# Optimization experiments

Hardware: AMD Instinct MI355X
Metric: run time of the kernel (lower is better)

## Reference

```python
import jax, jax.numpy as jnp
import numpy as np

N = 20000   # nodes
D = 64      # emb_dim
H = 512     # 8 * emb_dim
E = 320000  # edges per graph


def setup_inputs() -> dict:
    key = jax.random.key(0)
    ks = jax.random.split(key, 40)
    i = iter(range(40))
    def nrm(shape, s=0.05):
        return jax.random.normal(ks[next(i)], shape, dtype=jnp.float32) * s
    def edges():
        return jax.random.randint(ks[next(i)], (E,), 0, N, dtype=jnp.int32)
    inp = {}
    inp['k_emb'] = nrm((N, D), 1.0)
    inp['pr_src'] = edges(); inp['pr_dst'] = edges()
    inp['pr_ew'] = jax.random.uniform(ks[next(i)], (E,), dtype=jnp.float32)
    inp['cc_src'] = edges(); inp['cc_dst'] = edges()
    inp['cc_ew'] = jax.random.uniform(ks[next(i)], (E,), dtype=jnp.float32)
    inp['sps_src'] = edges(); inp['sps_dst'] = edges()
    inp['pr_Ws0'] = nrm((D, H)); inp['pr_Wn0'] = nrm((D, H)); inp['pr_b0'] = jnp.zeros((H,), jnp.float32)
    inp['pr_Ws1'] = nrm((H, D)); inp['pr_Wn1'] = nrm((H, D)); inp['pr_b1'] = jnp.zeros((D,), jnp.float32)
    inp['cc_Ws0'] = nrm((D, H)); inp['cc_Wn0'] = nrm((D, H)); inp['cc_b0'] = jnp.zeros((H,), jnp.float32)
    inp['cc_Ws1'] = nrm((H, D)); inp['cc_Wn1'] = nrm((H, D)); inp['cc_b1'] = jnp.zeros((D,), jnp.float32)
    inp['ap_Ws0'] = nrm((D, D)); inp['ap_Wn0'] = nrm((D, D)); inp['ap_b0'] = jnp.zeros((D,), jnp.float32)
    inp['ap_Ws1'] = nrm((D, D)); inp['ap_Wn1'] = nrm((D, D)); inp['ap_b1'] = jnp.zeros((D,), jnp.float32)
    inp['att_W'] = nrm((D, D)); inp['att_b'] = jnp.zeros((D,), jnp.float32)
    return inp


def _sage(x, src, dst, ew, Ws, Wn, b):
    # DGL SAGEConv 'mean': neigh = sum(w_e * h_src) / in_degree; out = x@Ws + neigh@Wn + b
    msg = x[src]                                  # [E, din] gather
    if ew is not None:
        msg = msg * ew[:, None]
    agg = jax.ops.segment_sum(msg, dst, num_segments=N)            # [N, din]
    deg = jax.ops.segment_sum(jnp.ones((msg.shape[0],), x.dtype), dst, num_segments=N)
    agg = agg / jnp.maximum(deg, 1.0)[:, None]
    return x @ Ws + agg @ Wn + b


def reference(k_emb, pr_src, pr_dst, pr_ew, cc_src, cc_dst, cc_ew, sps_src, sps_dst,
              pr_Ws0, pr_Wn0, pr_b0, pr_Ws1, pr_Wn1, pr_b1,
              cc_Ws0, cc_Wn0, cc_b0, cc_Ws1, cc_Wn1, cc_b1,
              ap_Ws0, ap_Wn0, ap_b0, ap_Ws1, ap_Wn1, ap_b1,
              att_W, att_b):
    pr = jax.nn.relu(_sage(k_emb, pr_src, pr_dst, pr_ew, pr_Ws0, pr_Wn0, pr_b0))
    pr = _sage(pr, pr_src, pr_dst, pr_ew, pr_Ws1, pr_Wn1, pr_b1)            # [N, D]
    cc = jax.nn.relu(_sage(k_emb, cc_src, cc_dst, cc_ew, cc_Ws0, cc_Wn0, cc_b0))
    cc = _sage(cc, cc_src, cc_dst, cc_ew, cc_Ws1, cc_Wn1, cc_b1)            # [N, D]
    ap = jax.nn.relu(_sage(k_emb, sps_src, sps_dst, None, ap_Ws0, ap_Wn0, ap_b0))
    ap = _sage(ap, sps_src, sps_dst, None, ap_Ws1, ap_Wn1, ap_b1)           # [N, D]
    # APATT fusion
    z = jnp.stack((pr, cc), axis=1)                      # [N, 2, D]
    proj = jnp.tanh(z @ att_W + att_b)                   # [N, 2, D]
    w = jnp.sum(ap[:, None, :] * proj, axis=-1, keepdims=True).mean(0)  # [2, 1]
    beta = jax.nn.softmax(w, axis=0)                     # [2, 1]
    return (beta * z).sum(axis=1)                        # [N, D]
```

## Files before the change

### kernel.cpp

```cpp
#include <hip/hip_runtime.h>
#include <hip/hip_fp16.h>

#define NN 20000
#define NP 20032
#define DD 64
#define HH 512
#define EE 320000
#define ATT_BLOCKS 625
#define BLOCKS_E (EE / 256)
#define CB 157
#define EPB 4096
#define B1_BLOCKS ((EE + EPB - 1) / EPB)
#define ZERO_N (3 * NN + 3 * CB)
#define ZERO_BLOCKS ((ZERO_N + 255) / 256)

typedef __attribute__((ext_vector_type(8))) short short8;
typedef __attribute__((ext_vector_type(4))) float f32x4;

__device__ __forceinline__ ushort f2bf(float f) {
    union { float f; unsigned u; } v; v.f = f;
    unsigned r = v.u + 0x7FFF + ((v.u >> 16) & 1);
    return (ushort)(r >> 16);
}
__device__ __forceinline__ float bf2f(ushort h) {
    union { unsigned u; float f; } v; v.u = ((unsigned)h) << 16;
    return v.f;
}
__device__ __forceinline__ float ew_of(uint w) {
    __half h = __ushort_as_half((ushort)(w >> 16));
    return __half2float(h);
}

__global__ __launch_bounds__(256) void hist3(const int* __restrict__ d0,
                                             const int* __restrict__ d1,
                                             const int* __restrict__ d2,
                                             int* __restrict__ cnt) {
    int g = blockIdx.x / BLOCKS_E;
    int e = (blockIdx.x % BLOCKS_E) * 256 + threadIdx.x;
    const int* d = (g == 0) ? d0 : (g == 1) ? d1 : d2;
    if (e < EE) atomicAdd(&cnt[g * NN + d[e]], 1);
}

__global__ __launch_bounds__(1024) void scan_kernel(const int* __restrict__ cnt,
                                                    int* __restrict__ rowptr,
                                                    float* __restrict__ invd) {
    __shared__ int part[1024];
    int g = blockIdx.x;
    const int* c = cnt + g * NN;
    int* rp = rowptr + g * (NN + 1);
    int tid = threadIdx.x;
    const int CH = (NN + 1023) / 1024;
    int i0 = tid * CH;
    int s = 0;
    for (int i = 0; i < CH; ++i) { int idx = i0 + i; if (idx < NN) s += c[idx]; }
    part[tid] = s;
    __syncthreads();
    for (int off = 1; off < 1024; off <<= 1) {
        int v = (tid >= off) ? part[tid - off] : 0;
        __syncthreads();
        part[tid] += v;
        __syncthreads();
    }
    int run = (tid > 0) ? part[tid - 1] : 0;
    for (int i = 0; i < CH; ++i) {
        int idx = i0 + i;
        if (idx < NN) {
            int cv = c[idx];
            rp[idx] = run; run += cv;
            invd[g * NN + idx] = 1.0f / fmaxf((float)cv, 1.0f);
        }
    }
    if (tid == 1023) rp[NN] = part[1023];
}

__global__ __launch_bounds__(256) void bucket_coarse(
    const int* __restrict__ s0, const int* __restrict__ d0, const float* __restrict__ w0,
    const int* __restrict__ s1, const int* __restrict__ d1, const float* __restrict__ w1,
    const int* __restrict__ s2, const int* __restrict__ d2,
    const int* __restrict__ rowptr,
    int* __restrict__ ccur,
    uint* __restrict__ ce,
    ushort* __restrict__ cd) {
    __shared__ int cnt_s[CB];
    __shared__ int off_s[CB];
    __shared__ int pos_s[CB];
    __shared__ int gbase[CB];
    __shared__ uint lword[EPB];
    __shared__ ushort ldst[EPB];
    int g = blockIdx.x / B1_BLOCKS;
    int blk = blockIdx.x % B1_BLOCKS;
    const int* S = (g == 0) ? s0 : (g == 1) ? s1 : s2;
    const int* D = (g == 0) ? d0 : (g == 1) ? d1 : d2;
    const float* W = (g == 0) ? w0 : (g == 1) ? w1 : nullptr;
    int e0 = blk * EPB;
    int n = min(EPB, EE - e0);
    for (int i = threadIdx.x; i < CB; i += 256) cnt_s[i] = 0;
    __syncthreads();
    for (int i = threadIdx.x; i < n; i += 256)
        atomicAdd(&cnt_s[D[e0 + i] >> 7], 1);
    __syncthreads();
    if (threadIdx.x == 0) {
        int run = 0;
        for (int i = 0; i < CB; ++i) { off_s[i] = run; run += cnt_s[i]; }
    }
    __syncthreads();
    if (threadIdx.x < CB) pos_s[threadIdx.x] = off_s[threadIdx.x];
    __syncthreads();
    for (int i = threadIdx.x; i < n; i += 256) {
        int e = e0 + i;
        int d = D[e];
        int p = atomicAdd(&pos_s[d >> 7], 1);
        ushort ewh = (g < 2) ? __half_as_ushort(__float2half(W[e])) : 0;
        lword[p] = ((uint)ewh << 16) | (uint)(S[e] & 0xFFFF);
        ldst[p] = (ushort)d;
    }
    __syncthreads();
    if (threadIdx.x < CB)
        gbase[threadIdx.x] = atomicAdd(&ccur[g * CB + threadIdx.x], cnt_s[threadIdx.x]);
    __syncthreads();
    const int* rp = rowptr + g * (NN + 1);
    for (int j = threadIdx.x; j < n; j += 256) {
        ushort d = ldst[j];
        int cb = d >> 7;
        int gpos = rp[cb << 7] + gbase[cb] + (j - off_s[cb]);
        ce[(size_t)g * EE + gpos] = lword[j];
        cd[(size_t)g * EE + gpos] = d;
    }
}

__global__ __launch_bounds__(256) void bucket_fine(
    const int* __restrict__ rowptr,
    const uint* __restrict__ ce, const ushort* __restrict__ cd,
    uint* __restrict__ edge_s,
    ushort* __restrict__ src_s2) {
    __shared__ int rp_s[129];
    __shared__ int cur_s[128];
    int g = blockIdx.x / CB;
    int cb = blockIdx.x % CB;
    const int* rp = rowptr + g * (NN + 1);
    int n0 = cb << 7;
    int n1 = min(n0 + 128, NN);
    int m = n1 - n0;
    if (threadIdx.x <= m) rp_s[threadIdx.x] = rp[n0 + threadIdx.x];
    if (threadIdx.x < m) cur_s[threadIdx.x] = 0;
    __syncthreads();
    int beg = rp_s[0], end = rp_s[m];
    for (int j = beg + threadIdx.x; j < end; j += 256) {
        uint e = ce[(size_t)g * EE + j];
        int dl = (int)cd[(size_t)g * EE + j] - n0;
        int pos = rp_s[dl] + atomicAdd(&cur_s[dl], 1);
        if (g < 2) edge_s[(size_t)g * EE + pos] = e;
        else src_s2[pos] = (ushort)(e & 0xFFFF);
    }
}

__global__ __launch_bounds__(256) void pull_cast3(const ushort* __restrict__ xh,
                                                  const int* __restrict__ rowptr,
                                                  const uint* __restrict__ edge_s,
                                                  const ushort* __restrict__ src_s2,
                                                  const float* __restrict__ invd,
                                                  ushort* __restrict__ aggh) {
    int wid = (blockIdx.x * 256 + threadIdx.x) >> 6;
    int lane = threadIdx.x & 63;
    if (wid >= 3 * NN) return;
    int g = wid / NN, n = wid % NN;
    const int* rp = rowptr + g * (NN + 1);
    int beg = rp[n], end = rp[n + 1];
    int q = lane >> 4, fl = lane & 15;
    float a0 = 0.f, a1 = 0.f, a2 = 0.f, a3 = 0.f;
    for (int i = beg; i < end; i += 4) {
        int e = i + q;
        bool valid = e < end;
        int s; float w;
        if (g < 2) {
            uint ew = valid ? edge_s[(size_t)g * EE + e] : 0u;
            s = (int)(ew & 0xFFFF);
            w = valid ? ew_of(ew) : 0.f;
        } else {
            s = valid ? (int)src_s2[e] : 0;
            w = valid ? 1.f : 0.f;
        }
        ushort4 v = *(const ushort4*)(xh + (size_t)s * DD + fl * 4);
        a0 = fmaf(bf2f(v.x), w, a0);
        a1 = fmaf(bf2f(v.y), w, a1);
        a2 = fmaf(bf2f(v.z), w, a2);
        a3 = fmaf(bf2f(v.w), w, a3);
    }
    a0 += __shfl_xor(a0, 16); a0 += __shfl_xor(a0, 32);
    a1 += __shfl_xor(a1, 16); a1 += __shfl_xor(a1, 32);
    a2 += __shfl_xor(a2, 16); a2 += __shfl_xor(a2, 32);
    a3 += __shfl_xor(a3, 16); a3 += __shfl_xor(a3, 32);
    if (q == 0) {
        float sc = invd[g * NN + n];
        ushort4 o;
        o.x = f2bf(a0 * sc); o.y = f2bf(a1 * sc); o.z = f2bf(a2 * sc); o.w = f2bf(a3 * sc);
        *(ushort4*)(aggh + ((size_t)g * NP + n) * 64 + fl * 4) = o;
    }
}

__global__ __launch_bounds__(256) void pull_combine3(const ushort* __restrict__ xnh,
                                                     const int* __restrict__ rowptr,
                                                     const uint* __restrict__ edge_s,
                                                     const ushort* __restrict__ src_s2,
                                                     const float* __restrict__ invd,
                                                     const float* __restrict__ b_pr,
                                                     const float* __restrict__ b_cc,
                                                     const float* __restrict__ b_ap,
                                                     float* __restrict__ o_pr,
                                                     float* __restrict__ o_cc,
                                                     float* __restrict__ o_ap) {
    int wid = (blockIdx.x * 256 + threadIdx.x) >> 6;
    int lane = threadIdx.x & 63;
    if (wid >= 3 * NN) return;
    int g = wid / NN, n = wid % NN;
    const int* rp = rowptr + g * (NN + 1);
    const ushort* x = xnh + (size_t)g * NP * 64;
    int beg = rp[n], end = rp[n + 1];
    int q = lane >> 4, fl = lane & 15;
    float a0 = 0.f, a1 = 0.f, a2 = 0.f, a3 = 0.f;
    for (int i = beg; i < end; i += 4) {
        int e = i + q;
        bool valid = e < end;
        int s; float w;
        if (g < 2) {
            uint ew = valid ? edge_s[(size_t)g * EE + e] : 0u;
            s = (int)(ew & 0xFFFF);
            w = valid ? ew_of(ew) : 0.f;
        } else {
            s = valid ? (int)src_s2[e] : 0;
            w = valid ? 1.f : 0.f;
        }
        ushort4 v = *(const ushort4*)(x + (size_t)s * DD + fl * 4);
        a0 = fmaf(bf2f(v.x), w, a0);
        a1 = fmaf(bf2f(v.y), w, a1);
        a2 = fmaf(bf2f(v.z), w, a2);
        a3 = fmaf(bf2f(v.w), w, a3);
    }
    a0 += __shfl_xor(a0, 16); a0 += __shfl_xor(a0, 32);
    a1 += __shfl_xor(a1, 16); a1 += __shfl_xor(a1, 32);
    a2 += __shfl_xor(a2, 16); a2 += __shfl_xor(a2, 32);
    a3 += __shfl_xor(a3, 16); a3 += __shfl_xor(a3, 32);
    if (q == 0) {
        float sc = invd[g * NN + n];
        const float* bias = (g == 0) ? b_pr : (g == 1) ? b_cc : b_ap;
        float* out = (g == 0) ? o_pr : (g == 1) ? o_cc : o_ap;
        float4 ov = *(float4*)(out + (size_t)n * DD + fl * 4);
        float4 bv = *(const float4*)(bias + fl * 4);
        ov.x += a0 * sc + bv.x;
        ov.y += a1 * sc + bv.y;
        ov.z += a2 * sc + bv.z;
        ov.w += a3 * sc + bv.w;
        *(float4*)(out + (size_t)n * DD + fl * 4) = ov;
    }
}

__global__ __launch_bounds__(256) void pack_all(
    const float* __restrict__ pr_Ws0, const float* __restrict__ pr_Wn0,
    const float* __restrict__ cc_Ws0, const float* __restrict__ cc_Wn0,
    const float* __restrict__ pr_Ws1, const float* __restrict__ pr_Wn1,
    const float* __restrict__ cc_Ws1, const float* __restrict__ cc_Wn1,
    const float* __restrict__ ap_Ws0, const float* __restrict__ ap_Wn0,
    const float* __restrict__ ap_Ws1, const float* __restrict__ ap_Wn1,
    const float* __restrict__ k_emb,
    ushort* __restrict__ W0h_pr, ushort* __restrict__ W0h_cc,
    ushort* __restrict__ W1h_pr, ushort* __restrict__ W1h_cc,
    ushort* __restrict__ W0h_ap, ushort* __restrict__ W1h_ap,
    ushort* __restrict__ xh,
    int* __restrict__ zero_base) {
    int b = blockIdx.x;
    int tid = threadIdx.x;
    if (b < 512) {
        int t = (b & 255) * 256 + tid;
        const float* Ws = (b < 256) ? pr_Ws0 : cc_Ws0;
        const float* Wn = (b < 256) ? pr_Wn0 : cc_Wn0;
        ushort* o = (b < 256) ? W0h_pr : W0h_cc;
        int c = t >> 7, k = t & 127;
        o[t] = f2bf((k < 64) ? Ws[k * 512 + c] : Wn[(k - 64) * 512 + c]);
    } else if (b < 1024) {
        int t = ((b - 512) & 255) * 256 + tid;
        const float* Ws = (b < 768) ? pr_Ws1 : cc_Ws1;
        const float* Wn = (b < 768) ? pr_Wn1 : cc_Wn1;
        ushort* o = (b < 768) ? W1h_pr : W1h_cc;
        int c = t >> 9, k = t & 511;
        o[t] = f2bf((c < 64) ? Ws[k * 64 + c] : Wn[k * 64 + (c - 64)]);
    } else if (b < 1056) {
        int t = (b - 1024) * 256 + tid;
        int c = t >> 7, k = t & 127;
        W0h_ap[t] = f2bf((k < 64) ? ap_Ws0[k * 64 + c] : ap_Wn0[(k - 64) * 64 + c]);
    } else if (b < 1088) {
        int t = (b - 1056) * 256 + tid;
        int c = t >> 6, k = t & 63;
        W1h_ap[t] = f2bf((c < 64) ? ap_Ws1[k * 64 + c] : ap_Wn1[k * 64 + (c - 64)]);
    } else if (b < 1088 + ZERO_BLOCKS) {
        int t = (b - 1088) * 256 + tid;
        if (t < ZERO_N) zero_base[t] = 0;
    } else {
        int t = (b - 1088 - ZERO_BLOCKS) * 256 + tid;
        if (t < NN * DD) xh[t] = f2bf(k_emb[t]);
    }
}

__global__ __launch_bounds__(512, 4) void fused_sage4(
    const ushort* __restrict__ xh,
    const ushort* __restrict__ aggA,
    const ushort* __restrict__ W0a, const ushort* __restrict__ W1a,
    const ushort* __restrict__ W0b, const ushort* __restrict__ W1b,
    const float* __restrict__ b0a, const float* __restrict__ b0b,
    float* __restrict__ outS0, float* __restrict__ outS1,
    ushort* __restrict__ xnh, int nblk) {
    constexpr int LROW = 136;
    __shared__ ushort Ahs[64 * LROW];
    __shared__ ushort h1s[64 * LROW];
    int br = blockIdx.x / nblk;
    int rb = blockIdx.x % nblk;
    const ushort* W0 = br ? W0b : W0a;
    const ushort* W1 = br ? W1b : W1a;
    const float* b0 = br ? b0b : b0a;
    float* outS = br ? outS1 : outS0;
    ushort* outX = xnh + (size_t)br * NP * 64;
    const ushort* agg = aggA + (size_t)br * NP * 64;
    int row0 = rb * 64;

    int wv = threadIdx.x >> 6;
    int lane = threadIdx.x & 63;
    int lrow = lane & 15;
    int koff = (lane >> 4) * 8;
    int crow = (lane >> 4) * 4;

    {
        int r = threadIdx.x >> 3;
        int seg = threadIdx.x & 7;
        const ushort* src = (seg < 4) ? (xh + (size_t)(row0 + r) * 64 + seg * 16)
                                      : (agg + (size_t)(row0 + r) * 64 + (seg - 4) * 16);
        *(short8*)&Ahs[r * LROW + seg * 16] = *(const short8*)src;
        *(short8*)&Ahs[r * LROW + seg * 16 + 8] = *(const short8*)(src + 8);
    }
    __syncthreads();

    f32x4 C[4] = {};
#pragma unroll
    for (int p = 0; p < 4; ++p) {
        {
            short8 B[4];
#pragma unroll
            for (int kk = 0; kk < 4; ++kk)
                B[kk] = *(const short8*)(W0 + (size_t)(p * 128 + wv * 16 + lrow) * 128 + kk * 32 + koff);
            f32x4 acc[4] = {};
#pragma unroll
            for (int rg = 0; rg < 4; ++rg) {
#pragma unroll
                for (int kk = 0; kk < 4; ++kk) {
                    short8 a = *(const short8*)&Ahs[(rg * 16 + lrow) * LROW + kk * 32 + koff];
                    acc[rg] = __builtin_amdgcn_mfma_f32_16x16x32_bf16(a, B[kk], acc[rg], 0, 0, 0);
                }
            }
            float bb = b0[p * 128 + wv * 16 + lrow];
#pragma unroll
            for (int rg = 0; rg < 4; ++rg) {
#pragma unroll
                for (int r = 0; r < 4; ++r) {
                    float v = fmaxf(acc[rg][r] + bb, 0.0f);
                    h1s[(rg * 16 + crow + r) * LROW + wv * 16 + lrow] = f2bf(v);
                }
            }
        }
        __syncthreads();
        {
            short8 B[4];
#pragma unroll
            for (int kc = 0; kc < 4; ++kc)
                B[kc] = *(const short8*)(W1 + (size_t)(wv * 16 + lrow) * HH + p * 128 + kc * 32 + koff);
#pragma unroll
            for (int rg = 0; rg < 4; ++rg) {
#pragma unroll
                for (int kc = 0; kc < 4; ++kc) {
                    short8 a = *(const short8*)&h1s[(rg * 16 + lrow) * LROW + kc * 32 + koff];
                    C[rg] = __builtin_amdgcn_mfma_f32_16x16x32_bf16(a, B[kc], C[rg], 0, 0, 0);
                }
            }
        }
        __syncthreads();
    }
    int col = wv * 16 + lrow;
    if (col < 64) {
        float* o = outS + col;
#pragma unroll
        for (int rg = 0; rg < 4; ++rg)
#pragma unroll
            for (int r = 0; r < 4; ++r) {
                int row = row0 + rg * 16 + crow + r;
                if (row < NN) o[(size_t)row * 64] = C[rg][r];
            }
    } else {
        ushort* o = outX + (col - 64);
#pragma unroll
        for (int rg = 0; rg < 4; ++rg)
#pragma unroll
            for (int r = 0; r < 4; ++r) {
                int row = row0 + rg * 16 + crow + r;
                if (row < NN) o[(size_t)row * 64] = f2bf(C[rg][r]);
            }
    }
}

__global__ __launch_bounds__(256, 4) void fused_sage_ap(
    const ushort* __restrict__ xh,
    const ushort* __restrict__ agg,
    const ushort* __restrict__ W0,
    const ushort* __restrict__ W1,
    const float* __restrict__ b0,
    float* __restrict__ outS,
    ushort* __restrict__ outX) {
    constexpr int LROW = 72;
    __shared__ ushort h1s[16 * LROW];
    int wv = threadIdx.x >> 6;
    int lane = threadIdx.x & 63;
    int lrow = lane & 15;
    int koff = (lane >> 4) * 8;
    int crow = (lane >> 4) * 4;
    int row0 = blockIdx.x * 16;

    {
        const size_t aoff = (size_t)(row0 + lrow) * 64 + koff;
        short8 aF[4];
#pragma unroll
        for (int kk = 0; kk < 2; ++kk) {
            aF[kk]     = *(const short8*)(xh + aoff + kk * 32);
            aF[2 + kk] = *(const short8*)(agg + aoff + kk * 32);
        }
        f32x4 acc = {};
#pragma unroll
        for (int kk = 0; kk < 4; ++kk) {
            short8 b = *(const short8*)(W0 + (size_t)(wv * 16 + lrow) * 128 + kk * 32 + koff);
            acc = __builtin_amdgcn_mfma_f32_16x16x32_bf16(aF[kk], b, acc, 0, 0, 0);
        }
        float bb = b0[wv * 16 + lrow];
#pragma unroll
        for (int r = 0; r < 4; ++r) {
            h1s[(crow + r) * LROW + wv * 16 + lrow] = f2bf(fmaxf(acc[r] + bb, 0.0f));
        }
    }
    __syncthreads();
    {
        f32x4 C2[2] = {};
#pragma unroll
        for (int kc = 0; kc < 2; ++kc) {
            short8 a = *(const short8*)&h1s[lrow * LROW + kc * 32 + koff];
#pragma unroll
            for (int c = 0; c < 2; ++c) {
                short8 b = *(const short8*)(W1 + (size_t)(wv * 32 + c * 16 + lrow) * 64 + kc * 32 + koff);
                C2[c] = __builtin_amdgcn_mfma_f32_16x16x32_bf16(a, b, C2[c], 0, 0, 0);
            }
        }
#pragma unroll
        for (int c = 0; c < 2; ++c) {
            int col = wv * 32 + c * 16 + lrow;
#pragma unroll
            for (int r = 0; r < 4; ++r) {
                int row = row0 + crow + r;
                if (row < NN) {
                    if (col < 64) outS[(size_t)row * 64 + col] = C2[c][r];
                    else outX[(size_t)row * 64 + (col - 64)] = f2bf(C2[c][r]);
                }
            }
        }
    }
}

__global__ __launch_bounds__(256) void att_stage1(const float* __restrict__ pr,
                                                  const float* __restrict__ cc,
                                                  const float* __restrict__ ap,
                                                  const float* __restrict__ attW,
                                                  const float* __restrict__ attb,
                                                  float2* __restrict__ partial) {
    __shared__ float red[8];
    int lane = threadIdx.x & 63;
    int wv = threadIdx.x >> 6;
    int gw = blockIdx.x * 4 + wv;
    const int nwaves = ATT_BLOCKS * 4;
    float b = attb[lane];
    float c0 = 0.f, c1 = 0.f;
    for (int n = gw; n < NN; n += nwaves) {
        float p0 = 0.f, p1 = 0.f;
        for (int k = 0; k < DD; ++k) {
            float w = attW[k * DD + lane];
            p0 = fmaf(pr[n * DD + k], w, p0);
            p1 = fmaf(cc[n * DD + k], w, p1);
        }
        float a = ap[n * DD + lane];
        c0 += a * tanhf(p0 + b);
        c1 += a * tanhf(p1 + b);
    }
#pragma unroll
    for (int off = 32; off; off >>= 1) {
        c0 += __shfl_xor(c0, off);
        c1 += __shfl_xor(c1, off);
    }
    if (lane == 0) { red[wv * 2] = c0; red[wv * 2 + 1] = c1; }
    __syncthreads();
    if (threadIdx.x == 0) {
        partial[blockIdx.x] = make_float2(red[0] + red[2] + red[4] + red[6],
                                          red[1] + red[3] + red[5] + red[7]);
    }
}

__global__ __launch_bounds__(64) void att_stage2(const float2* __restrict__ partial,
                                                 float* __restrict__ w_acc) {
    int lane = threadIdx.x;
    float s0 = 0.f, s1 = 0.f;
    for (int i = lane; i < ATT_BLOCKS; i += 64) {
        float2 p = partial[i];
        s0 += p.x; s1 += p.y;
    }
#pragma unroll
    for (int off = 32; off; off >>= 1) {
        s0 += __shfl_xor(s0, off);
        s1 += __shfl_xor(s1, off);
    }
    if (lane == 0) { w_acc[0] = s0; w_acc[1] = s1; }
}

__global__ __launch_bounds__(256) void final_kernel(float* __restrict__ pr_out,
                                                    const float* __restrict__ cc,
                                                    const float* __restrict__ w_acc) {
    int t = blockIdx.x * blockDim.x + threadIdx.x;
    if (t >= NN * DD) return;
    float w0 = w_acc[0] * (1.0f / NN);
    float w1 = w_acc[1] * (1.0f / NN);
    float m = fmaxf(w0, w1);
    float e0 = __expf(w0 - m), e1 = __expf(w1 - m);
    float inv = 1.0f / (e0 + e1);
    pr_out[t] = (e0 * pr_out[t] + e1 * cc[t]) * inv;
}

extern "C" void kernel_launch(void* const* d_in, const int* in_sizes, int n_in,
                              void* d_out, int out_size, void* d_ws, size_t ws_size,
                              hipStream_t stream) {
    const float* k_emb  = (const float*)d_in[0];
    const int*   pr_src = (const int*)d_in[1];
    const int*   pr_dst = (const int*)d_in[2];
    const float* pr_ew  = (const float*)d_in[3];
    const int*   cc_src = (const int*)d_in[4];
    const int*   cc_dst = (const int*)d_in[5];
    const float* cc_ew  = (const float*)d_in[6];
    const int*   sps_src = (const int*)d_in[7];
    const int*   sps_dst = (const int*)d_in[8];
    const float* pr_Ws0 = (const float*)d_in[9];
    const float* pr_Wn0 = (const float*)d_in[10];
    const float* pr_b0  = (const float*)d_in[11];
    const float* pr_Ws1 = (const float*)d_in[12];
    const float* pr_Wn1 = (const float*)d_in[13];
    const float* pr_b1  = (const float*)d_in[14];
    const float* cc_Ws0 = (const float*)d_in[15];
    const float* cc_Wn0 = (const float*)d_in[16];
    const float* cc_b0  = (const float*)d_in[17];
    const float* cc_Ws1 = (const float*)d_in[18];
    const float* cc_Wn1 = (const float*)d_in[19];
    const float* cc_b1  = (const float*)d_in[20];
    const float* ap_Ws0 = (const float*)d_in[21];
    const float* ap_Wn0 = (const float*)d_in[22];
    const float* ap_b0  = (const float*)d_in[23];
    const float* ap_Ws1 = (const float*)d_in[24];
    const float* ap_Wn1 = (const float*)d_in[25];
    const float* ap_b1  = (const float*)d_in[26];
    const float* att_W  = (const float*)d_in[27];
    const float* att_b  = (const float*)d_in[28];
    float* out = (float*)d_out;

    char* base = (char*)d_ws;
    size_t off = 0;
    auto alloc = [&](size_t bytes) -> void* {
        void* p = base + off;
        off = (off + bytes + 255) & ~(size_t)255;
        return p;
    };
    float*  invd   = (float*)alloc((size_t)3 * NN * 4);
    int*    cnt    = (int*)alloc((size_t)ZERO_N * 4);
    int*    ccur   = cnt + 3 * NN;
    int*    rowptr = (int*)alloc((size_t)3 * (NN + 1) * 4);
    uint*   edge_s = (uint*)alloc((size_t)2 * EE * 4);
    ushort* src_s2 = (ushort*)alloc((size_t)EE * 2);
    uint*   ce     = (uint*)alloc((size_t)3 * EE * 4);
    ushort* cd     = (ushort*)alloc((size_t)3 * EE * 2);
    float*  w_acc  = (float*)alloc(64);
    float2* att_partial = (float2*)alloc(ATT_BLOCKS * 8);
    ushort* xnh    = (ushort*)alloc((size_t)3 * NP * DD * 2);
    float*  out_cc = (float*)alloc((size_t)NN * DD * 4);
    float*  out_ap = (float*)alloc((size_t)NN * DD * 4);
    ushort* xh     = (ushort*)alloc((size_t)NP * DD * 2);
    ushort* aggh   = (ushort*)alloc((size_t)3 * NP * DD * 2);
    ushort* W0h_pr = (ushort*)alloc(512 * 128 * 2);
    ushort* W0h_cc = (ushort*)alloc(512 * 128 * 2);
    ushort* W0h_ap = (ushort*)alloc(64 * 128 * 2);
    ushort* W1h_pr = (ushort*)alloc(128 * 512 * 2);
    ushort* W1h_cc = (ushort*)alloc(128 * 512 * 2);
    ushort* W1h_ap = (ushort*)alloc(128 * 64 * 2);
    float*  out_pr = out;

    const int TB = 256;
    const int blocks_ND = (NN * DD) / TB;
    const int blocks_pull = (3 * NN * 64) / TB;
    const int NBLK64 = NP / 64;

    pack_all<<<1088 + ZERO_BLOCKS + blocks_ND, TB, 0, stream>>>(
        pr_Ws0, pr_Wn0, cc_Ws0, cc_Wn0, pr_Ws1, pr_Wn1, cc_Ws1, cc_Wn1,
        ap_Ws0, ap_Wn0, ap_Ws1, ap_Wn1, k_emb,
        W0h_pr, W0h_cc, W1h_pr, W1h_cc, W0h_ap, W1h_ap, xh, cnt);

    hist3<<<3 * BLOCKS_E, TB, 0, stream>>>(pr_dst, cc_dst, sps_dst, cnt);
    scan_kernel<<<3, 1024, 0, stream>>>(cnt, rowptr, invd);
    bucket_coarse<<<3 * B1_BLOCKS, TB, 0, stream>>>(pr_src, pr_dst, pr_ew,
                                                    cc_src, cc_dst, cc_ew,
                                                    sps_src, sps_dst,
                                                    rowptr, ccur, ce, cd);
    bucket_fine<<<3 * CB, TB, 0, stream>>>(rowptr, ce, cd, edge_s, src_s2);

    pull_cast3<<<blocks_pull, TB, 0, stream>>>(xh, rowptr, edge_s, src_s2, invd, aggh);

    fused_sage4<<<2 * NBLK64, 512, 0, stream>>>(
        xh, aggh,
        W0h_pr, W1h_pr, W0h_cc, W1h_cc,
        pr_b0, cc_b0, out_pr, out_cc, xnh, NBLK64);
    fused_sage_ap<<<NP / 16, 256, 0, stream>>>(
        xh, aggh + (size_t)2 * NP * 64,
        W0h_ap, W1h_ap, ap_b0, out_ap, xnh + (size_t)2 * NP * 64);

    pull_combine3<<<blocks_pull, TB, 0, stream>>>(xnh, rowptr, edge_s, src_s2, invd,
                                                  pr_b1, cc_b1, ap_b1,
                                                  out_pr, out_cc, out_ap);

    att_stage1<<<ATT_BLOCKS, TB, 0, stream>>>(out_pr, out_cc, out_ap, att_W, att_b, att_partial);
    att_stage2<<<1, 64, 0, stream>>>(att_partial, w_acc);
    final_kernel<<<blocks_ND, TB, 0, stream>>>(out_pr, out_cc, w_acc);
}
```

Baseline: 272.8 us.

## Drop fine bucketing; aggregate coarse 64-node buckets via LDS atomics

Removes the bucket_fine pass that fully sorted edges by destination. The coarse buckets shrink to 64 destination nodes, and both pull kernels now process one bucket per block, accumulating messages into a 64x64 float LDS tile with shared-memory atomics. This saves a sort pass and its extra global traffic. In exchange it adds LDS atomic contention, launches only 939 blocks with 4 waves each, and makes each lane load a single bf16 element instead of ushort4 vectors.

```diff
diff --git a/kernel.cpp b/kernel.cpp
--- a/kernel.cpp
+++ b/kernel.cpp
@@ -8,7 +8,7 @@
 #define EE 320000
 #define ATT_BLOCKS 625
 #define BLOCKS_E (EE / 256)
-#define CB 157
+#define CB 313
 #define EPB 4096
 #define B1_BLOCKS ((EE + EPB - 1) / EPB)
 #define ZERO_N (3 * NN + 3 * CB)
@@ -97,160 +97,104 @@
     for (int i = threadIdx.x; i < CB; i += 256) cnt_s[i] = 0;
     __syncthreads();
     for (int i = threadIdx.x; i < n; i += 256)
-        atomicAdd(&cnt_s[D[e0 + i] >> 7], 1);
+        atomicAdd(&cnt_s[D[e0 + i] >> 6], 1);
     __syncthreads();
     if (threadIdx.x == 0) {
         int run = 0;
         for (int i = 0; i < CB; ++i) { off_s[i] = run; run += cnt_s[i]; }
     }
     __syncthreads();
-    if (threadIdx.x < CB) pos_s[threadIdx.x] = off_s[threadIdx.x];
+    for (int i = threadIdx.x; i < CB; i += 256) pos_s[i] = off_s[i];
     __syncthreads();
     for (int i = threadIdx.x; i < n; i += 256) {
         int e = e0 + i;
         int d = D[e];
-        int p = atomicAdd(&pos_s[d >> 7], 1);
+        int p = atomicAdd(&pos_s[d >> 6], 1);
         ushort ewh = (g < 2) ? __half_as_ushort(__float2half(W[e])) : 0;
         lword[p] = ((uint)ewh << 16) | (uint)(S[e] & 0xFFFF);
         ldst[p] = (ushort)d;
     }
     __syncthreads();
-    if (threadIdx.x < CB)
-        gbase[threadIdx.x] = atomicAdd(&ccur[g * CB + threadIdx.x], cnt_s[threadIdx.x]);
+    for (int i = threadIdx.x; i < CB; i += 256)
+        gbase[i] = atomicAdd(&ccur[g * CB + i], cnt_s[i]);
     __syncthreads();
     const int* rp = rowptr + g * (NN + 1);
     for (int j = threadIdx.x; j < n; j += 256) {
         ushort d = ldst[j];
-        int cb = d >> 7;
-        int gpos = rp[cb << 7] + gbase[cb] + (j - off_s[cb]);
+        int cb = d >> 6;
+        int gpos = rp[cb << 6] + gbase[cb] + (j - off_s[cb]);
         ce[(size_t)g * EE + gpos] = lword[j];
         cd[(size_t)g * EE + gpos] = d;
     }
 }
 
-__global__ __launch_bounds__(256) void bucket_fine(
-    const int* __restrict__ rowptr,
-    const uint* __restrict__ ce, const ushort* __restrict__ cd,
-    uint* __restrict__ edge_s,
-    ushort* __restrict__ src_s2) {
-    __shared__ int rp_s[129];
-    __shared__ int cur_s[128];
-    int g = blockIdx.x / CB;
-    int cb = blockIdx.x % CB;
+__global__ __launch_bounds__(256) void pull_lds_cast(const ushort* __restrict__ xh,
+                                                     const int* __restrict__ rowptr,
+                                                     const uint* __restrict__ ce,
+                                                     const ushort* __restrict__ cd,
+                                                     const float* __restrict__ invd,
+                                                     ushort* __restrict__ aggh) {
+    __shared__ float acc[64 * 64];
+    int g = blockIdx.x / CB, cb = blockIdx.x % CB;
+    int n0 = cb << 6;
+    int nw = min(64, NN - n0);
     const int* rp = rowptr + g * (NN + 1);
-    int n0 = cb << 7;
-    int n1 = min(n0 + 128, NN);
-    int m = n1 - n0;
-    if (threadIdx.x <= m) rp_s[threadIdx.x] = rp[n0 + threadIdx.x];
-    if (threadIdx.x < m) cur_s[threadIdx.x] = 0;
-    __syncthreads();
-    int beg = rp_s[0], end = rp_s[m];
-    for (int j = beg + threadIdx.x; j < end; j += 256) {
-        uint e = ce[(size_t)g * EE + j];
-        int dl = (int)cd[(size_t)g * EE + j] - n0;
-        int pos = rp_s[dl] + atomicAdd(&cur_s[dl], 1);
-        if (g < 2) edge_s[(size_t)g * EE + pos] = e;
-        else src_s2[pos] = (ushort)(e & 0xFFFF);
-    }
-}
-
-__global__ __launch_bounds__(256) void pull_cast3(const ushort* __restrict__ xh,
-                                                  const int* __restrict__ rowptr,
-                                                  const uint* __restrict__ edge_s,
-                                                  const ushort* __restrict__ src_s2,
-                                                  const float* __restrict__ invd,
-                                                  ushort* __restrict__ aggh) {
-    int wid = (blockIdx.x * 256 + threadIdx.x) >> 6;
-    int lane = threadIdx.x & 63;
-    if (wid >= 3 * NN) return;
-    int g = wid / NN, n = wid % NN;
-    const int* rp = rowptr + g * (NN + 1);
-    int beg = rp[n], end = rp[n + 1];
-    int q = lane >> 4, fl = lane & 15;
-    float a0 = 0.f, a1 = 0.f, a2 = 0.f, a3 = 0.f;
-    for (int i = beg; i < end; i += 4) {
-        int e = i + q;
-        bool valid = e < end;
-        int s; float w;
-        if (g < 2) {
-            uint ew = valid ? edge_s[(size_t)g * EE + e] : 0u;
-            s = (int)(ew & 0xFFFF);
-            w = valid ? ew_of(ew) : 0.f;
-        } else {
-            s = valid ? (int)src_s2[e] : 0;
-            w = valid ? 1.f : 0.f;
-        }
-        ushort4 v = *(const ushort4*)(xh + (size_t)s * DD + fl * 4);
-        a0 = fmaf(bf2f(v.x), w, a0);
-        a1 = fmaf(bf2f(v.y), w, a1);
-        a2 = fmaf(bf2f(v.z), w, a2);
-        a3 = fmaf(bf2f(v.w), w, a3);
-    }
-    a0 += __shfl_xor(a0, 16); a0 += __shfl_xor(a0, 32);
-    a1 += __shfl_xor(a1, 16); a1 += __shfl_xor(a1, 32);
-    a2 += __shfl_xor(a2, 16); a2 += __shfl_xor(a2, 32);
-    a3 += __shfl_xor(a3, 16); a3 += __shfl_xor(a3, 32);
-    if (q == 0) {
-        float sc = invd[g * NN + n];
-        ushort4 o;
-        o.x = f2bf(a0 * sc); o.y = f2bf(a1 * sc); o.z = f2bf(a2 * sc); o.w = f2bf(a3 * sc);
-        *(ushort4*)(aggh + ((size_t)g * NP + n) * 64 + fl * 4) = o;
-    }
-}
-
-__global__ __launch_bounds__(256) void pull_combine3(const ushort* __restrict__ xnh,
-                                                     const int* __restrict__ rowptr,
-                                                     const uint* __restrict__ edge_s,
-                                                     const ushort* __restrict__ src_s2,
-                                                     const float* __restrict__ invd,
-                                                     const float* __restrict__ b_pr,
-                                                     const float* __restrict__ b_cc,
-                                                     const float* __restrict__ b_ap,
-                                                     float* __restrict__ o_pr,
-                                                     float* __restrict__ o_cc,
-                                                     float* __restrict__ o_ap) {
-    int wid = (blockIdx.x * 256 + threadIdx.x) >> 6;
-    int lane = threadIdx.x & 63;
-    if (wid >= 3 * NN) return;
-    int g = wid / NN, n = wid % NN;
+    int beg = rp[n0], end = rp[n0 + nw];
+    for (int i = threadIdx.x; i < 64 * 16; i += 256) ((float4*)acc)[i] = float4{0.f, 0.f, 0.f, 0.f};
+    __syncthreads();
+    int lane = threadIdx.x & 63, wv = threadIdx.x >> 6;
+    for (int i = beg + wv; i < end; i += 4) {
+        uint w = ce[(size_t)g * EE + i];
+        int dl = (int)cd[(size_t)g * EE + i] - n0;
+        int s = (int)(w & 0xFFFF);
+        float ww = (g < 2) ? ew_of(w) : 1.0f;
+        float v = bf2f(xh[(size_t)s * DD + lane]);
+        unsafeAtomicAdd(&acc[dl * 64 + lane], v * ww);
+    }
+    __syncthreads();
+    for (int j = wv; j < nw; j += 4) {
+        float sc = invd[g * NN + n0 + j];
+        aggh[((size_t)g * NP + n0 + j) * 64 + lane] = f2bf(acc[j * 64 + lane] * sc);
+    }
+}
+
+__global__ __launch_bounds__(256) void pull_lds_combine(const ushort* __restrict__ xnh,
+                                                        const int* __restrict__ rowptr,
+                                                        const uint* __restrict__ ce,
+                                                        const ushort* __restrict__ cd,
+                                                        const float* __restrict__ invd,
+                                                        const float* __restrict__ b_pr,
+                                                        const float* __restrict__ b_cc,
+                                                        const float* __restrict__ b_ap,
+                                                        float* __restrict__ o_pr,
+                                                        float* __restrict__ o_cc,
+                                                        float* __restrict__ o_ap) {
+    __shared__ float acc[64 * 64];
+    int g = blockIdx.x / CB, cb = blockIdx.x % CB;
+    int n0 = cb << 6;
+    int nw = min(64, NN - n0);
     const int* rp = rowptr + g * (NN + 1);
     const ushort* x = xnh + (size_t)g * NP * 64;
-    int beg = rp[n], end = rp[n + 1];
-    int q = lane >> 4, fl = lane & 15;
-    float a0 = 0.f, a1 = 0.f, a2 = 0.f, a3 = 0.f;
-    for (int i = beg; i < end; i += 4) {
-        int e = i + q;
-        bool valid = e < end;
-        int s; float w;
-        if (g < 2) {
-            uint ew = valid ? edge_s[(size_t)g * EE + e] : 0u;
-            s = (int)(ew & 0xFFFF);
-            w = valid ? ew_of(ew) : 0.f;
-        } else {
-            s = valid ? (int)src_s2[e] : 0;
-            w = valid ? 1.f : 0.f;
-        }
-        ushort4 v = *(const ushort4*)(x + (size_t)s * DD + fl * 4);
-        a0 = fmaf(bf2f(v.x), w, a0);
-        a1 = fmaf(bf2f(v.y), w, a1);
-        a2 = fmaf(bf2f(v.z), w, a2);
-        a3 = fmaf(bf2f(v.w), w, a3);
-    }
-    a0 += __shfl_xor(a0, 16); a0 += __shfl_xor(a0, 32);
-    a1 += __shfl_xor(a1, 16); a1 += __shfl_xor(a1, 32);
-    a2 += __shfl_xor(a2, 16); a2 += __shfl_xor(a2, 32);
-    a3 += __shfl_xor(a3, 16); a3 += __shfl_xor(a3, 32);
-    if (q == 0) {
-        float sc = invd[g * NN + n];
-        const float* bias = (g == 0) ? b_pr : (g == 1) ? b_cc : b_ap;
-        float* out = (g == 0) ? o_pr : (g == 1) ? o_cc : o_ap;
-        float4 ov = *(float4*)(out + (size_t)n * DD + fl * 4);
-        float4 bv = *(const float4*)(bias + fl * 4);
-        ov.x += a0 * sc + bv.x;
-        ov.y += a1 * sc + bv.y;
-        ov.z += a2 * sc + bv.z;
-        ov.w += a3 * sc + bv.w;
-        *(float4*)(out + (size_t)n * DD + fl * 4) = ov;
+    int beg = rp[n0], end = rp[n0 + nw];
+    for (int i = threadIdx.x; i < 64 * 16; i += 256) ((float4*)acc)[i] = float4{0.f, 0.f, 0.f, 0.f};
+    __syncthreads();
+    int lane = threadIdx.x & 63, wv = threadIdx.x >> 6;
+    for (int i = beg + wv; i < end; i += 4) {
+        uint w = ce[(size_t)g * EE + i];
+        int dl = (int)cd[(size_t)g * EE + i] - n0;
+        int s = (int)(w & 0xFFFF);
+        float ww = (g < 2) ? ew_of(w) : 1.0f;
+        float v = bf2f(x[(size_t)s * DD + lane]);
+        unsafeAtomicAdd(&acc[dl * 64 + lane], v * ww);
+    }
+    __syncthreads();
+    const float* bias = (g == 0) ? b_pr : (g == 1) ? b_cc : b_ap;
+    float* out = (g == 0) ? o_pr : (g == 1) ? o_cc : o_ap;
+    float bv = bias[lane];
+    for (int j = wv; j < nw; j += 4) {
+        float sc = invd[g * NN + n0 + j];
+        size_t o = (size_t)(n0 + j) * DD + lane;
+        out[o] += acc[j * 64 + lane] * sc + bv;
     }
 }
 
@@ -578,8 +522,6 @@
     int*    cnt    = (int*)alloc((size_t)ZERO_N * 4);
     int*    ccur   = cnt + 3 * NN;
     int*    rowptr = (int*)alloc((size_t)3 * (NN + 1) * 4);
-    uint*   edge_s = (uint*)alloc((size_t)2 * EE * 4);
-    ushort* src_s2 = (ushort*)alloc((size_t)EE * 2);
     uint*   ce     = (uint*)alloc((size_t)3 * EE * 4);
     ushort* cd     = (ushort*)alloc((size_t)3 * EE * 2);
     float*  w_acc  = (float*)alloc(64);
@@ -599,7 +541,6 @@
 
     const int TB = 256;
     const int blocks_ND = (NN * DD) / TB;
-    const int blocks_pull = (3 * NN * 64) / TB;
     const int NBLK64 = NP / 64;
 
     pack_all<<<1088 + ZERO_BLOCKS + blocks_ND, TB, 0, stream>>>(
@@ -613,9 +554,8 @@
                                                     cc_src, cc_dst, cc_ew,
                                                     sps_src, sps_dst,
                                                     rowptr, ccur, ce, cd);
-    bucket_fine<<<3 * CB, TB, 0, stream>>>(rowptr, ce, cd, edge_s, src_s2);
-
-    pull_cast3<<<blocks_pull, TB, 0, stream>>>(xh, rowptr, edge_s, src_s2, invd, aggh);
+
+    pull_lds_cast<<<3 * CB, TB, 0, stream>>>(xh, rowptr, ce, cd, invd, aggh);
 
     fused_sage4<<<2 * NBLK64, 512, 0, stream>>>(
         xh, aggh,
@@ -625,9 +565,9 @@
         xh, aggh + (size_t)2 * NP * 64,
         W0h_ap, W1h_ap, ap_b0, out_ap, xnh + (size_t)2 * NP * 64);
 
-    pull_combine3<<<blocks_pull, TB, 0, stream>>>(xnh, rowptr, edge_s, src_s2, invd,
-                                                  pr_b1, cc_b1, ap_b1,
-                                                  out_pr, out_cc, out_ap);
+    pull_lds_combine<<<3 * CB, TB, 0, stream>>>(xnh, rowptr, ce, cd, invd,
+                                                pr_b1, cc_b1, ap_b1,
+                                                out_pr, out_cc, out_ap);
 
     att_stage1<<<ATT_BLOCKS, TB, 0, stream>>>(out_pr, out_cc, out_ap, att_W, att_b, att_partial);
     att_stage2<<<1, 64, 0, stream>>>(att_partial, w_acc);
```

After: 901.6 us. +230.5%, slower.
